# Performance work log

Measured on AMD Instinct MI355X. Metric: run time of the kernel, lower is better.

Reference implementation:

```python
import jax, jax.numpy as jnp
import numpy as np

SCORE_THRESHOLD = 0.5
IOU_THRESHOLD = 0.5
N = 8192
IMG = 640.0


def setup_inputs() -> dict:
    key = jax.random.key(0)
    k1, k2, k3 = jax.random.split(key, 3)
    # valid xyxy boxes on a 640px canvas: x2 > x1, y2 > y1
    xy1 = jax.random.uniform(k1, (N, 2), dtype=jnp.float32) * (IMG - 64.0)
    wh = jax.random.uniform(k2, (N, 2), dtype=jnp.float32) * 96.0 + 4.0
    xyxy = jnp.concatenate([xy1, xy1 + wh], axis=1)  # [N,4]
    person_conf = jax.random.uniform(k3, (N,), dtype=jnp.float32)  # [N]
    return {"xyxy": xyxy, "person_conf": person_conf}


def _pairwise_iou(boxes):
    # boxes: [N,4] xyxy -> iou: [N,N]
    x1, y1, x2, y2 = boxes[:, 0], boxes[:, 1], boxes[:, 2], boxes[:, 3]
    area = (x2 - x1) * (y2 - y1)  # [N]
    ix1 = jnp.maximum(x1[:, None], x1[None, :])
    iy1 = jnp.maximum(y1[:, None], y1[None, :])
    ix2 = jnp.minimum(x2[:, None], x2[None, :])
    iy2 = jnp.minimum(y2[:, None], y2[None, :])
    iw = jnp.maximum(ix2 - ix1, 0.0)
    ih = jnp.maximum(iy2 - iy1, 0.0)
    inter = iw * ih
    union = area[:, None] + area[None, :] - inter
    return inter / jnp.maximum(union, 1e-9)


def reference(xyxy, person_conf):
    # score-threshold filter (as a mask to stay jit-compatible / fixed shape)
    valid = person_conf >= SCORE_THRESHOLD  # [N]
    # sort by score descending; invalid boxes sink to the bottom
    sort_scores = jnp.where(valid, person_conf, -jnp.inf)
    order = jnp.argsort(-sort_scores)  # [N]
    boxes_s = xyxy[order]              # [N,4]
    scores_s = person_conf[order]      # [N]
    valid_s = valid[order]             # [N]

    iou = _pairwise_iou(boxes_s)  # [N,N]
    idx = jnp.arange(N)

    def body(i, keep):
        # box i (if still kept) suppresses lower-scored overlapping boxes
        sup = keep[i] & (iou[i] > IOU_THRESHOLD) & (idx > i)
        return keep & ~sup

    keep = jax.lax.fori_loop(0, N, body, valid_s)  # [N] bool

    boxes_and_scores = jnp.concatenate([boxes_s, scores_s[:, None]], axis=1)  # [N,5]
    out = jnp.where(keep[:, None], boxes_and_scores, 0.0)  # suppressed rows zeroed
    return out, keep
```

## Files before the change

kernel.cpp:

```cpp
#include <hip/hip_runtime.h>

typedef unsigned long long u64;
typedef unsigned int u32;
typedef unsigned short u16;

static constexpr int N = 8192;
static constexpr int NW = N / 64;
static constexpr int RSEG = 32;
static constexpr int CAPW = 512;
static constexpr int ECAP = 9216;


__device__ __forceinline__ u64 make_key(float s, int i) {
  u32 adj = (s >= 0.5f) ? (__float_as_uint(s) + 1u) : 0u;
  return ((u64)adj << 32) | (u64)(u32)(N - 1 - i);
}

__global__ __launch_bounds__(256)
void rank_kernel(const float* __restrict__ conf, u32* __restrict__ rank_partial,
                 u32* __restrict__ cntG, u64* __restrict__ validmG,
                 int* __restrict__ nvG) {
  __shared__ u64 sk[256];
  const int t = threadIdx.x;
  if (blockIdx.x == 0 && blockIdx.y == 0) {
    if (t < NW) { cntG[t] = 0; validmG[t] = 0; }
    if (t == 0) *nvG = 0;
  }
  const int jb = blockIdx.y;
  const int j = jb * 256 + t;
  sk[t] = make_key(conf[j], j);
  __syncthreads();
  const int i = blockIdx.x * 256 + t;
  const u64 ki = make_key(conf[i], i);
  int cnt = 0;
  #pragma unroll 8
  for (int k = 0; k < 256; ++k) cnt += (sk[k] > ki);
  rank_partial[jb * N + i] = (u32)cnt;
}

__global__ __launch_bounds__(256)
void scatter_kernel(const float4* __restrict__ xyxy, const float* __restrict__ conf,
                    const u32* __restrict__ rank_partial,
                    float4* __restrict__ boxes_s, float* __restrict__ scores_s,
                    float* __restrict__ areas_s, u64* __restrict__ validmG,
                    int* __restrict__ nvG) {
  #pragma clang fp contract(off)
  const int i = blockIdx.x * 256 + threadIdx.x;
  u32 r = 0;
  #pragma unroll
  for (int jb = 0; jb < RSEG; ++jb) r += rank_partial[jb * N + i];
  float4 b = xyxy[i];
  float c = conf[i];
  boxes_s[r] = b;
  scores_s[r] = c;
  areas_s[r] = (b.z - b.x) * (b.w - b.y);
  if (c >= 0.5f) {
    atomicOr(&validmG[r >> 6], 1ull << (r & 63));
    atomicAdd(nvG, 1);
  }
}

__global__ __launch_bounds__(256)
void mask_kernel(const float4* __restrict__ boxes_s, const float* __restrict__ areas_s,
                 const float* __restrict__ scores_s,
                 uint4* __restrict__ edge4, u32* __restrict__ cntG,
                 u64* __restrict__ Dg) {
  #pragma clang fp contract(off)
  __shared__ float4 cb[4][64];
  __shared__ float ca[4][64];
  const int wave = threadIdx.x >> 6;
  const int t = threadIdx.x & 63;
  const int xb = blockIdx.x * 4 + wave;
  const int yb = blockIdx.y;
  if (xb < yb) return;
  if (scores_s[xb * 64] < 0.5f) return;
  cb[wave][t] = boxes_s[xb * 64 + t];
  ca[wave][t] = areas_s[xb * 64 + t];
  const int i = yb * 64 + t;
  const float4 rb = boxes_s[i];
  const float ra = areas_s[i];
  const float sc_i = scores_s[i];
  const int jbase = xb * 64;
  u64 w = 0;
  for (int q = 0; q < 64; ++q) {
    float4 c = cb[wave][q];
    float ix1 = fmaxf(rb.x, c.x);
    float iy1 = fmaxf(rb.y, c.y);
    float ix2 = fminf(rb.z, c.z);
    float iy2 = fminf(rb.w, c.w);
    float iw = fmaxf(ix2 - ix1, 0.0f);
    float ih = fmaxf(iy2 - iy1, 0.0f);
    float inter = iw * ih;
    float uni = fmaxf((ra + ca[wave][q]) - inter, 1e-9f);
    float iou = inter / uni;
    if ((iou > 0.5f) && (jbase + q > i)) w |= (1ull << q);
  }
  if (sc_i < 0.5f) w = 0;
  if (xb == yb) {
    Dg[(u64)yb * 64 + t] = w;
    return;
  }
  u64 nz = __ballot(w != 0ull);
  if (!nz) return;
  int base = 0;
  if (t == 0) base = atomicAdd(&cntG[yb], (u32)__popcll(nz));
  base = __shfl(base, 0);
  if (w) {
    int idx = base + __popcll(nz & ((1ull << t) - 1ull));
    if (idx < CAPW) {
      edge4[(u64)yb * CAPW + idx] =
          make_uint4((u32)w, (u32)(w >> 32), (u32)i | ((u32)xb << 16), 0u);
    }
  }
}

__global__ __launch_bounds__(256, 1)
void sweep_kernel(const uint4* __restrict__ edge4, const u32* __restrict__ cntG,
                  const u64* __restrict__ validmG, const int* __restrict__ nvG,
                  const u64* __restrict__ Dg, u64* __restrict__ keepmG) {
  __shared__ u64 maskL[ECAP];
  __shared__ u64 D[NW * 64];
  __shared__ u16 metaL[ECAP];
  __shared__ u64 rem64[NW];
  __shared__ u64 keepL[NW];
  __shared__ u64 validL[NW];
  __shared__ u32 offL[NW + 1];
  __shared__ u32 cntL[NW];
  const int tid = threadIdx.x;
  const int t = tid & 63;

  if (tid < NW) {
    cntL[tid] = min(cntG[tid], (u32)CAPW);
    rem64[tid] = 0;
    keepL[tid] = 0;
    validL[tid] = validmG[tid];
  }
  __syncthreads();

  if (tid < 64) {
    u32 a = cntL[t];
    u32 b = cntL[64 + t];
    #pragma unroll
    for (int d = 1; d < 64; d <<= 1) { u32 n = __shfl_up(a, d); if (t >= d) a += n; }
    u32 tot = __shfl(a, 63);
    #pragma unroll
    for (int d = 1; d < 64; d <<= 1) { u32 n = __shfl_up(b, d); if (t >= d) b += n; }
    b += tot;
    a = min(a, (u32)ECAP);
    b = min(b, (u32)ECAP);
    if (t == 0) offL[0] = 0;
    offL[1 + t] = a;
    offL[65 + t] = b;
  }
  for (int s = tid; s < NW * 64; s += 256) D[s] = Dg[s];
  __syncthreads();

  const u32 T = offL[NW];
  for (u32 s = tid; s < T; s += 256) {
    int lo = 0, hi = NW;
    #pragma unroll
    for (int it = 0; it < 7; ++it) {
      int mid = (lo + hi) >> 1;
      if (offL[mid] <= s) lo = mid; else hi = mid;
    }
    uint4 r = edge4[(u64)lo * CAPW + (s - offL[lo])];
    maskL[s] = ((u64)r.y << 32) | (u64)r.x;
    metaL[s] = (u16)((r.z & 63u) | ((r.z >> 16) << 6));
  }
  __syncthreads();

  if (tid < 64) {
    const int NWv = min((*nvG + 63) >> 6, NW);
    u32 o_cur = offL[0];
    u32 oe_cur = offL[1];
    for (int y = 0; y < NWv; ++y) {
      u64 rm = rem64[y];
      u64 dcur = D[y * 64 + t];
      u64 vv = validL[y];
      const u32 o = o_cur;
      const u32 ce = oe_cur - o;
      o_cur = oe_cur;
      oe_cur = offL[(y + 2 <= NW) ? (y + 2) : NW];
      u32 mt0 = 0, mt1 = 0, mt2 = 0, mt3 = 0, mt4 = 0, mt5 = 0, mt6 = 0, mt7 = 0;
      u64 mm0 = 0, mm1 = 0, mm2 = 0, mm3 = 0, mm4 = 0, mm5 = 0, mm6 = 0, mm7 = 0;
      bool v0 = (u32)t < ce, v1 = 64u + t < ce, v2 = 128u + t < ce, v3 = 192u + t < ce;
      bool v4 = false, v5 = false, v6 = false, v7 = false;
      if (v0) { mt0 = metaL[o + t];        mm0 = maskL[o + t]; }
      if (v1) { mt1 = metaL[o + 64 + t];   mm1 = maskL[o + 64 + t]; }
      if (v2) { mt2 = metaL[o + 128 + t];  mm2 = maskL[o + 128 + t]; }
      if (v3) { mt3 = metaL[o + 192 + t];  mm3 = maskL[o + 192 + t]; }
      if (ce > 256) {
        v4 = 256u + t < ce; v5 = 320u + t < ce; v6 = 384u + t < ce; v7 = 448u + t < ce;
        if (v4) { mt4 = metaL[o + 256 + t]; mm4 = maskL[o + 256 + t]; }
        if (v5) { mt5 = metaL[o + 320 + t]; mm5 = maskL[o + 320 + t]; }
        if (v6) { mt6 = metaL[o + 384 + t]; mm6 = maskL[o + 384 + t]; }
        if (v7) { mt7 = metaL[o + 448 + t]; mm7 = maskL[o + 448 + t]; }
      }
      u64 kk = vv & ~rm;
      u64 im = __ballot(dcur != 0ull) & kk;
      while (im) {
        int q = __ffsll((long long)im) - 1;
        u64 dq = D[y * 64 + q];
        kk &= ~dq;
        im &= ~(1ull << q);
        im &= kk;
      }
      if (t == 0) keepL[y] = kk;
      if (v0 && ((kk >> (mt0 & 63u)) & 1ull)) atomicOr(&rem64[mt0 >> 6], mm0);
      if (v1 && ((kk >> (mt1 & 63u)) & 1ull)) atomicOr(&rem64[mt1 >> 6], mm1);
      if (v2 && ((kk >> (mt2 & 63u)) & 1ull)) atomicOr(&rem64[mt2 >> 6], mm2);
      if (v3 && ((kk >> (mt3 & 63u)) & 1ull)) atomicOr(&rem64[mt3 >> 6], mm3);
      if (ce > 256) {
        if (v4 && ((kk >> (mt4 & 63u)) & 1ull)) atomicOr(&rem64[mt4 >> 6], mm4);
        if (v5 && ((kk >> (mt5 & 63u)) & 1ull)) atomicOr(&rem64[mt5 >> 6], mm5);
        if (v6 && ((kk >> (mt6 & 63u)) & 1ull)) atomicOr(&rem64[mt6 >> 6], mm6);
        if (v7 && ((kk >> (mt7 & 63u)) & 1ull)) atomicOr(&rem64[mt7 >> 6], mm7);
      }
    }
  }
  __syncthreads();
  if (tid < NW) keepmG[tid] = keepL[tid];
}

__global__ __launch_bounds__(256)
void writeout_kernel(const u64* __restrict__ keepmG,
                     const float4* __restrict__ boxes_s,
                     const float* __restrict__ scores_s,
                     float* __restrict__ out) {
  const int s = blockIdx.x * 256 + threadIdx.x;
  bool keep = (keepmG[s >> 6] >> (s & 63)) & 1ull;
  float4 b = boxes_s[s];
  float sc = scores_s[s];
  float* row = out + (u64)s * 5;
  if (keep) {
    row[0] = b.x; row[1] = b.y; row[2] = b.z; row[3] = b.w; row[4] = sc;
    out[N * 5 + s] = 1.0f;
  } else {
    row[0] = 0.0f; row[1] = 0.0f; row[2] = 0.0f; row[3] = 0.0f; row[4] = 0.0f;
    out[N * 5 + s] = 0.0f;
  }
}

extern "C" void kernel_launch(void* const* d_in, const int* in_sizes, int n_in,
                              void* d_out, int out_size, void* d_ws, size_t ws_size,
                              hipStream_t stream) {
  const float4* xyxy = (const float4*)d_in[0];
  const float* conf  = (const float*)d_in[1];
  char* ws = (char*)d_ws;
  float4* boxes_s   = (float4*)(ws + 0);
  float*  scores_s  = (float*)(ws + 131072);
  float*  areas_s   = (float*)(ws + 163840);
  u32*    cntG      = (u32*)(ws + 196608);
  int*    nvG       = (int*)(ws + 197120);
  u64*    validmG   = (u64*)(ws + 197184);
  u64*    keepmG    = (u64*)(ws + 198208);
  u64*    Dg        = (u64*)(ws + 199680);
  uint4*  edge4     = (uint4*)(ws + 265216);
  u32*    rank_partial = (u32*)(ws + 1313792);
  float*  out       = (float*)d_out;

  dim3 rg(N / 256, RSEG);
  rank_kernel<<<rg, 256, 0, stream>>>(conf, rank_partial, cntG, validmG, nvG);
  scatter_kernel<<<N / 256, 256, 0, stream>>>(xyxy, conf, rank_partial,
                                              boxes_s, scores_s, areas_s,
                                              validmG, nvG);
  dim3 mg(NW / 4, NW);
  mask_kernel<<<mg, 256, 0, stream>>>(boxes_s, areas_s, scores_s,
                                      edge4, cntG, Dg);
  sweep_kernel<<<1, 256, 0, stream>>>(edge4, cntG, validmG, nvG, Dg, keepmG);
  writeout_kernel<<<N / 256, 256, 0, stream>>>(keepmG, boxes_s, scores_s, out);
}
```

Measured before the change: 139.2 us.

## Stream edge lists from global with register prefetch and transposed diagonal masks

The sweep kernel no longer stages the whole compacted edge list and diagonal masks into LDS with a prefix scan and binary search. Instead it reads each row-block's edges straight from global memory into registers, prefetching two blocks ahead in a three-slot rotation. The mask kernel now stores the diagonal block transposed (column masks) plus a per-block source bitmap, so the intra-block suppression loop becomes a ballot over register data rather than LDS reads. This removes the serial staging prologue but puts global-load latency on the sequential path, which relies on the prefetch to hide it; blocks with more than 256 edges take an unprefetched global loop.

```diff
diff --git a/kernel.cpp b/kernel.cpp
--- a/kernel.cpp
+++ b/kernel.cpp
@@ -2,13 +2,11 @@
 
 typedef unsigned long long u64;
 typedef unsigned int u32;
-typedef unsigned short u16;
 
 static constexpr int N = 8192;
 static constexpr int NW = N / 64;
 static constexpr int RSEG = 32;
 static constexpr int CAPW = 512;
-static constexpr int ECAP = 9216;
 
 
 __device__ __forceinline__ u64 make_key(float s, int i) {
@@ -64,7 +62,7 @@
 void mask_kernel(const float4* __restrict__ boxes_s, const float* __restrict__ areas_s,
                  const float* __restrict__ scores_s,
                  uint4* __restrict__ edge4, u32* __restrict__ cntG,
-                 u64* __restrict__ Dg) {
+                 u64* __restrict__ Cg, u64* __restrict__ srcG) {
   #pragma clang fp contract(off)
   __shared__ float4 cb[4][64];
   __shared__ float ca[4][64];
@@ -97,7 +95,14 @@
   }
   if (sc_i < 0.5f) w = 0;
   if (xb == yb) {
-    Dg[(u64)yb * 64 + t] = w;
+    u64 srcb = __ballot(w != 0ull);
+    u64 c = 0;
+    for (int l = 0; l < 64; ++l) {
+      u64 bl = __ballot(((w >> l) & 1ull) != 0ull);
+      if (t == l) c = bl;
+    }
+    Cg[(u64)yb * 64 + t] = c;
+    if (t == 0) srcG[yb] = srcb;
     return;
   }
   u64 nz = __ballot(w != 0ull);
@@ -114,17 +119,59 @@
   }
 }
 
+#define STEP(Pa, Pc)                                                          \
+  do {                                                                        \
+    if (y >= NWv) goto done;                                                  \
+    int yl = y + 2; if (yl > NW - 1) yl = NW - 1;                             \
+    const uint4* pp = edge4 + (u64)yl * CAPW;                                 \
+    Pc##0 = pp[t]; Pc##1 = pp[64 + t];                                        \
+    Pc##2 = pp[128 + t]; Pc##3 = pp[192 + t];                                 \
+    Pc##C = Cg[(u64)yl * 64 + t];                                             \
+    Pc##S = srcG[yl];                                                         \
+    Pc##N = cntL[yl];                                                         \
+    u64 rm = rem64[y];                                                        \
+    u64 kk = validL[y] & ~rm;                                                 \
+    u64 S = (Pa##S) & kk;                                                     \
+    while (S) {                                                               \
+      int q = __ffsll((long long)S) - 1;                                      \
+      u64 V = __ballot((((Pa##C) >> q) & 1ull) != 0ull);                      \
+      kk &= ~V;                                                               \
+      S &= ~(1ull << q);                                                      \
+      S &= kk;                                                                \
+    }                                                                         \
+    if (t == 0) keepL[y] = kk;                                                \
+    u32 ce = (Pa##N);                                                         \
+    if ((u32)t < ce && ((kk >> ((Pa##0).z & 63u)) & 1ull))                    \
+      atomicOr(&rem64[(Pa##0).z >> 16],                                       \
+               ((u64)(Pa##0).y << 32) | (u64)(Pa##0).x);                      \
+    if (64u + (u32)t < ce && ((kk >> ((Pa##1).z & 63u)) & 1ull))              \
+      atomicOr(&rem64[(Pa##1).z >> 16],                                       \
+               ((u64)(Pa##1).y << 32) | (u64)(Pa##1).x);                      \
+    if (128u + (u32)t < ce && ((kk >> ((Pa##2).z & 63u)) & 1ull))             \
+      atomicOr(&rem64[(Pa##2).z >> 16],                                       \
+               ((u64)(Pa##2).y << 32) | (u64)(Pa##2).x);                      \
+    if (192u + (u32)t < ce && ((kk >> ((Pa##3).z & 63u)) & 1ull))             \
+      atomicOr(&rem64[(Pa##3).z >> 16],                                       \
+               ((u64)(Pa##3).y << 32) | (u64)(Pa##3).x);                      \
+    if (ce > 256u) {                                                          \
+      const uint4* ps = edge4 + (u64)y * CAPW;                                \
+      for (u32 s = 256u + (u32)t; s < ce; s += 64u) {                         \
+        uint4 rr = ps[s];                                                     \
+        if ((kk >> (rr.z & 63u)) & 1ull)                                      \
+          atomicOr(&rem64[rr.z >> 16], ((u64)rr.y << 32) | (u64)rr.x);        \
+      }                                                                       \
+    }                                                                         \
+    ++y;                                                                      \
+  } while (0)
+
 __global__ __launch_bounds__(256, 1)
 void sweep_kernel(const uint4* __restrict__ edge4, const u32* __restrict__ cntG,
                   const u64* __restrict__ validmG, const int* __restrict__ nvG,
-                  const u64* __restrict__ Dg, u64* __restrict__ keepmG) {
-  __shared__ u64 maskL[ECAP];
-  __shared__ u64 D[NW * 64];
-  __shared__ u16 metaL[ECAP];
+                  const u64* __restrict__ Cg, const u64* __restrict__ srcG,
+                  u64* __restrict__ keepmG) {
   __shared__ u64 rem64[NW];
   __shared__ u64 keepL[NW];
   __shared__ u64 validL[NW];
-  __shared__ u32 offL[NW + 1];
   __shared__ u32 cntL[NW];
   const int tid = threadIdx.x;
   const int t = tid & 63;
@@ -138,89 +185,30 @@
   __syncthreads();
 
   if (tid < 64) {
-    u32 a = cntL[t];
-    u32 b = cntL[64 + t];
-    #pragma unroll
-    for (int d = 1; d < 64; d <<= 1) { u32 n = __shfl_up(a, d); if (t >= d) a += n; }
-    u32 tot = __shfl(a, 63);
-    #pragma unroll
-    for (int d = 1; d < 64; d <<= 1) { u32 n = __shfl_up(b, d); if (t >= d) b += n; }
-    b += tot;
-    a = min(a, (u32)ECAP);
-    b = min(b, (u32)ECAP);
-    if (t == 0) offL[0] = 0;
-    offL[1 + t] = a;
-    offL[65 + t] = b;
-  }
-  for (int s = tid; s < NW * 64; s += 256) D[s] = Dg[s];
-  __syncthreads();
-
-  const u32 T = offL[NW];
-  for (u32 s = tid; s < T; s += 256) {
-    int lo = 0, hi = NW;
-    #pragma unroll
-    for (int it = 0; it < 7; ++it) {
-      int mid = (lo + hi) >> 1;
-      if (offL[mid] <= s) lo = mid; else hi = mid;
-    }
-    uint4 r = edge4[(u64)lo * CAPW + (s - offL[lo])];
-    maskL[s] = ((u64)r.y << 32) | (u64)r.x;
-    metaL[s] = (u16)((r.z & 63u) | ((r.z >> 16) << 6));
-  }
-  __syncthreads();
-
-  if (tid < 64) {
     const int NWv = min((*nvG + 63) >> 6, NW);
-    u32 o_cur = offL[0];
-    u32 oe_cur = offL[1];
-    for (int y = 0; y < NWv; ++y) {
-      u64 rm = rem64[y];
-      u64 dcur = D[y * 64 + t];
-      u64 vv = validL[y];
-      const u32 o = o_cur;
-      const u32 ce = oe_cur - o;
-      o_cur = oe_cur;
-      oe_cur = offL[(y + 2 <= NW) ? (y + 2) : NW];
-      u32 mt0 = 0, mt1 = 0, mt2 = 0, mt3 = 0, mt4 = 0, mt5 = 0, mt6 = 0, mt7 = 0;
-      u64 mm0 = 0, mm1 = 0, mm2 = 0, mm3 = 0, mm4 = 0, mm5 = 0, mm6 = 0, mm7 = 0;
-      bool v0 = (u32)t < ce, v1 = 64u + t < ce, v2 = 128u + t < ce, v3 = 192u + t < ce;
-      bool v4 = false, v5 = false, v6 = false, v7 = false;
-      if (v0) { mt0 = metaL[o + t];        mm0 = maskL[o + t]; }
-      if (v1) { mt1 = metaL[o + 64 + t];   mm1 = maskL[o + 64 + t]; }
-      if (v2) { mt2 = metaL[o + 128 + t];  mm2 = maskL[o + 128 + t]; }
-      if (v3) { mt3 = metaL[o + 192 + t];  mm3 = maskL[o + 192 + t]; }
-      if (ce > 256) {
-        v4 = 256u + t < ce; v5 = 320u + t < ce; v6 = 384u + t < ce; v7 = 448u + t < ce;
-        if (v4) { mt4 = metaL[o + 256 + t]; mm4 = maskL[o + 256 + t]; }
-        if (v5) { mt5 = metaL[o + 320 + t]; mm5 = maskL[o + 320 + t]; }
-        if (v6) { mt6 = metaL[o + 384 + t]; mm6 = maskL[o + 384 + t]; }
-        if (v7) { mt7 = metaL[o + 448 + t]; mm7 = maskL[o + 448 + t]; }
-      }
-      u64 kk = vv & ~rm;
-      u64 im = __ballot(dcur != 0ull) & kk;
-      while (im) {
-        int q = __ffsll((long long)im) - 1;
-        u64 dq = D[y * 64 + q];
-        kk &= ~dq;
-        im &= ~(1ull << q);
-        im &= kk;
-      }
-      if (t == 0) keepL[y] = kk;
-      if (v0 && ((kk >> (mt0 & 63u)) & 1ull)) atomicOr(&rem64[mt0 >> 6], mm0);
-      if (v1 && ((kk >> (mt1 & 63u)) & 1ull)) atomicOr(&rem64[mt1 >> 6], mm1);
-      if (v2 && ((kk >> (mt2 & 63u)) & 1ull)) atomicOr(&rem64[mt2 >> 6], mm2);
-      if (v3 && ((kk >> (mt3 & 63u)) & 1ull)) atomicOr(&rem64[mt3 >> 6], mm3);
-      if (ce > 256) {
-        if (v4 && ((kk >> (mt4 & 63u)) & 1ull)) atomicOr(&rem64[mt4 >> 6], mm4);
-        if (v5 && ((kk >> (mt5 & 63u)) & 1ull)) atomicOr(&rem64[mt5 >> 6], mm5);
-        if (v6 && ((kk >> (mt6 & 63u)) & 1ull)) atomicOr(&rem64[mt6 >> 6], mm6);
-        if (v7 && ((kk >> (mt7 & 63u)) & 1ull)) atomicOr(&rem64[mt7 >> 6], mm7);
-      }
-    }
+    uint4 A0, A1, A2, A3, B0, B1, B2, B3, X0, X1, X2, X3;
+    u64 AC, BC, XC, AS, BS, XS;
+    u32 AN, BN, XN;
+    {
+      const uint4* pp = edge4;
+      A0 = pp[t]; A1 = pp[64 + t]; A2 = pp[128 + t]; A3 = pp[192 + t];
+      AC = Cg[t]; AS = srcG[0]; AN = cntL[0];
+      const uint4* pq = edge4 + (u64)CAPW;
+      B0 = pq[t]; B1 = pq[64 + t]; B2 = pq[128 + t]; B3 = pq[192 + t];
+      BC = Cg[64 + t]; BS = srcG[1]; BN = cntL[1];
+    }
+    int y = 0;
+    for (;;) {
+      STEP(A, X);
+      STEP(B, A);
+      STEP(X, B);
+    }
+done: ;
   }
   __syncthreads();
   if (tid < NW) keepmG[tid] = keepL[tid];
 }
+#undef STEP
 
 __global__ __launch_bounds__(256)
 void writeout_kernel(const u64* __restrict__ keepmG,
@@ -254,9 +242,10 @@
   int*    nvG       = (int*)(ws + 197120);
   u64*    validmG   = (u64*)(ws + 197184);
   u64*    keepmG    = (u64*)(ws + 198208);
-  u64*    Dg        = (u64*)(ws + 199680);
-  uint4*  edge4     = (uint4*)(ws + 265216);
-  u32*    rank_partial = (u32*)(ws + 1313792);
+  u64*    srcG      = (u64*)(ws + 199232);
+  u64*    Cg        = (u64*)(ws + 200704);
+  uint4*  edge4     = (uint4*)(ws + 266240);
+  u32*    rank_partial = (u32*)(ws + 1314816);
   float*  out       = (float*)d_out;
 
   dim3 rg(N / 256, RSEG);
@@ -266,7 +255,8 @@
                                               validmG, nvG);
   dim3 mg(NW / 4, NW);
   mask_kernel<<<mg, 256, 0, stream>>>(boxes_s, areas_s, scores_s,
-                                      edge4, cntG, Dg);
-  sweep_kernel<<<1, 256, 0, stream>>>(edge4, cntG, validmG, nvG, Dg, keepmG);
+                                      edge4, cntG, Cg, srcG);
+  sweep_kernel<<<1, 256, 0, stream>>>(edge4, cntG, validmG, nvG, Cg, srcG,
+                                      keepmG);
   writeout_kernel<<<N / 256, 256, 0, stream>>>(keepmG, boxes_s, scores_s, out);
 }
```

Measured after the change: 118.3 us. 15.0% less time.
